# Kernel tuning notes

Measured on AMD Instinct MI355X. Metric: run time of the kernel, lower is better.

## Reference

```python
import jax, jax.numpy as jnp
import numpy as np

N, E = 50000, 500000
DH, DL = 13, 128          # handcrafted / learned node feature dims
OH, OL = 32, 96           # node-encoder output dims; node_dim D = OH+OL
D = OH + OL               # 128
EIN = (DH + DL) + 1 + 3 * D + 1  # 527, forced by concat in forward
H = 256                   # MLP hidden width
HC = 64                   # classifier hidden width
EPS = 1e-8


def _mlp(x, W1, b1, W2, b2):
    # 2-layer MLP with ReLU, matching repo MLP(fc_dims=[H, out])
    return jax.nn.relu(x @ W1 + b1) @ W2 + b2


def _cosine(a, b):
    # torch.nn.CosineSimilarity(dim=1, eps=1e-8)
    na = jnp.maximum(jnp.linalg.norm(a, axis=-1), EPS)
    nb = jnp.maximum(jnp.linalg.norm(b, axis=-1), EPS)
    return jnp.sum(a * b, axis=-1) / (na * nb)


def _lin(key, fan_in, fan_out):
    kW, kb = jax.random.split(key)
    s = 1.0 / np.sqrt(fan_in)
    return (jax.random.uniform(kW, (fan_in, fan_out), jnp.float32, -s, s),
            jax.random.uniform(kb, (fan_out,), jnp.float32, -s, s))


def setup_inputs() -> dict:
    key = jax.random.key(0)
    ks = jax.random.split(key, 16)
    x1 = jax.random.normal(ks[0], (N, DH), jnp.float32)
    x2 = jax.random.normal(ks[1], (N, DL), jnp.float32)
    edge_index = jax.random.randint(ks[2], (2, E), 0, N, jnp.int64)
    Wh1, bh1 = _lin(ks[3], DH, H);   Wh2, bh2 = _lin(ks[4], H, OH)
    Wl1, bl1 = _lin(ks[5], DL, H);   Wl2, bl2 = _lin(ks[6], H, OL)
    We1, be1 = _lin(ks[7], EIN, H);  We2, be2 = _lin(ks[8], H, D)
    Wmsg, bmsg = _lin(ks[9], 2 * D, D)
    Wnode, bnode = _lin(ks[10], 2 * D, D)
    Wmp1, bmp1 = _lin(ks[11], 3 * D, H); Wmp2, bmp2 = _lin(ks[12], H, D)
    Wc1, bc1 = _lin(ks[13], D, HC);  Wc2, bc2 = _lin(ks[14], HC, 1)
    return dict(x1=x1, x2=x2, edge_index=edge_index,
                Wh1=Wh1, bh1=bh1, Wh2=Wh2, bh2=bh2,
                Wl1=Wl1, bl1=bl1, Wl2=Wl2, bl2=bl2,
                We1=We1, be1=be1, We2=We2, be2=be2,
                Wmsg=Wmsg, bmsg=bmsg, Wnode=Wnode, bnode=bnode,
                Wmp1=Wmp1, bmp1=bmp1, Wmp2=Wmp2, bmp2=bmp2,
                Wc1=Wc1, bc1=bc1, Wc2=Wc2, bc2=bc2)


def reference(x1, x2, edge_index,
              Wh1, bh1, Wh2, bh2,
              Wl1, bl1, Wl2, bl2,
              We1, be1, We2, be2,
              Wmsg, bmsg, Wnode, bnode,
              Wmp1, bmp1, Wmp2, bmp2,
              Wc1, bc1, Wc2, bc2):
    src, trg = edge_index[0], edge_index[1]
    # raw-feature edge descriptors
    x_init = jnp.concatenate((x1, x2), axis=-1)            # [N, 141]
    xi_s, xi_t = x_init[src], x_init[trg]                  # gathers [E, 141]
    sim1 = _cosine(xi_s, xi_t)                             # [E]
    abs_init = jnp.abs(xi_s - xi_t)                        # [E, 141]
    # node encoders
    h1 = _mlp(x1, Wh1, bh1, Wh2, bh2)                      # [N, 32]
    h2 = _mlp(x2, Wl1, bl1, Wl2, bl2)                      # [N, 96]
    x = jnp.concatenate((h1, h2), axis=-1)                 # [N, 128]
    xs, xt = x[src], x[trg]                                # [E, 128]
    sim2 = _cosine(xs, xt)                                 # [E]
    edge_feat_in = jnp.concatenate(
        (abs_init, sim1[:, None], xs, xt, jnp.abs(xs - xt), sim2[:, None]),
        axis=-1)                                           # [E, 527]
    e = _mlp(edge_feat_in, We1, be1, We2, be2)             # [E, 128]
    # edge MPNN round: edge->node aggregation, node update, edge update
    msg = jax.nn.relu(jnp.concatenate((xs, e), axis=-1) @ Wmsg + bmsg)  # [E, 128]
    agg = jax.ops.segment_sum(msg, trg, num_segments=N)    # [N, 128]
    xn = jax.nn.relu(jnp.concatenate((x, agg), axis=-1) @ Wnode + bnode)  # [N, 128]
    e_mp = _mlp(jnp.concatenate((xn[src], xn[trg], e), axis=-1),
                Wmp1, bmp1, Wmp2, bmp2)                    # [E, 128]
    pred = _mlp(e_mp, Wc1, bc1, Wc2, bc2)                  # [E, 1]
    return jnp.squeeze(pred, axis=-1)                      # [E]
```

## Files before the change

### kernel.cpp

```cpp
#include <hip/hip_runtime.h>
#include <hip/hip_bf16.h>
#include <hip/hip_fp16.h>


using fp16 = __half;
typedef _Float16 h16;
typedef _Float16 f16x8 __attribute__((ext_vector_type(8)));
typedef _Float16 h16x2 __attribute__((ext_vector_type(2)));
typedef short s16x8 __attribute__((ext_vector_type(8)));
typedef float f32x4 __attribute__((ext_vector_type(4)));

#define NN 50000
#define EE 500000
#define EPSC 1e-8f
#define SCAN_B 196

__device__ __forceinline__ float reluf(float v){ return v > 0.f ? v : 0.f; }

__device__ __forceinline__ float dot8(const f16x8 a, const f16x8 b, float acc)
{
#pragma unroll
  for (int i = 0; i < 4; ++i) {
    const h16x2 av = {a[2 * i], a[2 * i + 1]};
    const h16x2 bv = {b[2 * i], b[2 * i + 1]};
    acc = __builtin_amdgcn_fdot2(av, bv, acc, false);
  }
  return acc;
}

__device__ __forceinline__ f16x8 absdiff8(const f16x8 a, const f16x8 b)
{
  const f16x8 d = a - b;
  s16x8 di = __builtin_bit_cast(s16x8, d);
  di &= (short)0x7fff;
  return __builtin_bit_cast(f16x8, di);
}

#define OFF_E1   0
#define OFF_E2   139264
#define OFF_MSG  172032
#define OFF_NODE 204800
#define OFF_MP1  237568
#define OFF_MP2  335872
#define OFF_C1   368640
#define OFF_N1   376832
#define OFF_N2   458752
#define WT_TOTAL 524288
#define BF_TOTAL 640

__global__ __launch_bounds__(256) void k_prep(
    const float* __restrict__ We1, const float* __restrict__ We2,
    const float* __restrict__ Wmsg, const float* __restrict__ Wnode,
    const float* __restrict__ Wmp1, const float* __restrict__ Wmp2,
    const float* __restrict__ Wc1,
    const float* __restrict__ Wh1, const float* __restrict__ Wl1,
    const float* __restrict__ Wh2, const float* __restrict__ Wl2,
    const float* __restrict__ bh1, const float* __restrict__ bl1,
    const float* __restrict__ bh2, const float* __restrict__ bl2,
    h16* __restrict__ WT, float* __restrict__ BF)
{
  int idx = blockIdx.x * 256 + threadIdx.x;
  if (idx >= WT_TOTAL) {
    const int b = idx - WT_TOTAL;
    if (b < 512) BF[b] = (b < 256) ? bh1[b] : bl1[b - 256];
    else if (b < BF_TOTAL) {
      const int c = b - 512;
      BF[b] = (c < 32) ? bh2[c] : bl2[c - 32];
    }
    return;
  }
  h16 v;
  if (idx < OFF_E2) {
    const int L = idx, n = L / 544, k = L % 544;
    int r;
    if      (k < 128) r = 142 + k;
    else if (k < 256) r = 270 + (k - 128);
    else if (k < 384) r = 398 + (k - 256);
    else if (k < 512) r = 13 + (k - 384);
    else if (k < 525) r = k - 512;
    else if (k == 528) r = 141;
    else if (k == 529) r = 526;
    else r = -1;
    v = (h16)((r >= 0) ? We1[r * 256 + n] : 0.f);
  } else if (idx < OFF_MSG) {
    const int L = idx - OFF_E2, n = L >> 8, k = L & 255;
    v = (h16)We2[k * 128 + n];
  } else if (idx < OFF_NODE) {
    const int L = idx - OFF_MSG, n = L >> 8, k = L & 255;
    const int ko = (k < 128) ? (128 + k) : (k - 128);
    v = (h16)Wmsg[ko * 128 + n];
  } else if (idx < OFF_MP1) {
    const int L = idx - OFF_NODE, n = L >> 8, k = L & 255;
    v = (h16)Wnode[k * 128 + n];
  } else if (idx < OFF_MP2) {
    const int L = idx - OFF_MP1, n = L / 384, k = L % 384;
    v = (h16)Wmp1[k * 256 + n];
  } else if (idx < OFF_C1) {
    const int L = idx - OFF_MP2, n = L >> 8, k = L & 255;
    v = (h16)Wmp2[k * 128 + n];
  } else if (idx < OFF_N1) {
    const int L = idx - OFF_C1, n = L >> 7, k = L & 127;
    v = (h16)Wc1[k * 64 + n];
  } else if (idx < OFF_N2) {
    const int L = idx - OFF_N1, n = L / 160, k = L % 160;
    float f = 0.f;
    if (n < 256) { if (k < 13) f = Wh1[k * 256 + n]; }
    else { if (k >= 16 && k < 144) f = Wl1[(k - 16) * 256 + (n - 256)]; }
    v = (h16)f;
  } else {
    const int L = idx - OFF_N2, n = L >> 9, k = L & 511;
    float f = 0.f;
    if (n < 32) { if (k < 256) f = Wh2[k * 32 + n]; }
    else { if (k >= 256) f = Wl2[(k - 256) * 96 + (n - 32)]; }
    v = (h16)f;
  }
  WT[idx] = v;
}

__global__ __launch_bounds__(256) void k_cvt(
    const float* __restrict__ x1, const float* __restrict__ x2,
    const int* __restrict__ ei,
    h16* __restrict__ X1P, h16* __restrict__ X2H, int* __restrict__ CNT)
{
  const int idx = blockIdx.x * 256 + threadIdx.x;
  if (idx < EE) atomicAdd(&CNT[ei[EE + idx]], 1);
  if (idx < NN * 16) {
    const int nn = idx >> 4, j = idx & 15;
    X1P[idx] = (h16)((j < 13) ? x1[nn * 13 + j] : 0.f);
  }
  const int i2 = idx - NN * 16;
  if (i2 >= 0 && i2 < NN * 128) X2H[i2] = (h16)x2[i2];
}

__global__ __launch_bounds__(256) void k_scanA(
    const int* __restrict__ CNT, int* __restrict__ TEX, int* __restrict__ BS)
{
  __shared__ int sd[256];
  const int tid = threadIdx.x;
  const int i = blockIdx.x * 256 + tid;
  const int v = (i < NN) ? CNT[i] : 0;
  sd[tid] = v;
  __syncthreads();
  for (int off = 1; off < 256; off <<= 1) {
    const int x = (tid >= off) ? sd[tid - off] : 0;
    __syncthreads();
    sd[tid] += x;
    __syncthreads();
  }
  if (i < NN) TEX[i] = sd[tid] - v;
  if (tid == 255) BS[blockIdx.x] = sd[255];
}

__global__ __launch_bounds__(256) void k_scanB(
    const int* __restrict__ BS, int* __restrict__ BSSE)
{
  __shared__ int sd[256];
  const int tid = threadIdx.x;
  const int v = (tid < SCAN_B) ? BS[tid] : 0;
  sd[tid] = v;
  __syncthreads();
  for (int off = 1; off < 256; off <<= 1) {
    const int x = (tid >= off) ? sd[tid - off] : 0;
    __syncthreads();
    sd[tid] += x;
    __syncthreads();
  }
  if (tid < SCAN_B) BSSE[tid] = sd[tid] - v;
}

__global__ __launch_bounds__(256) void k_scatter(
    const int* __restrict__ ei, const int* __restrict__ TEX,
    const int* __restrict__ BSSE, int* __restrict__ POS,
    int* __restrict__ ES, int* __restrict__ ET, int* __restrict__ OID)
{
  const int e = blockIdx.x * 256 + threadIdx.x;
  if (e >= EE) return;
  const int t = ei[EE + e];
  const int p = atomicAdd(&POS[t], 1);
  const int idx = BSSE[t >> 8] + TEX[t] + p;
  ES[idx] = ei[e];
  ET[idx] = t;
  OID[idx] = e;
}

template<int ROWS, int UDIM, int KP, int LDA, int WAVES, int RS, bool RELU,
         bool ENDSYNC, typename F>
__device__ __forceinline__ void mfma_gemm(const h16* sA,
    const h16* __restrict__ WT, const float* __restrict__ bias, F emit)
{
  constexpr int CS = WAVES / RS;
  constexpr int RG = ROWS / RS;
  constexpr int RT = RG / 16;
  constexpr int NPW0 = UDIM / CS;
  constexpr int NPW = (NPW0 < 16) ? 16 : NPW0;
  constexpr int NT = NPW / 16;
  constexpr int NSTEPS = KP / 32;
  constexpr int CH0 = (NT >= 8) ? 1 : ((NT >= 4) ? 2 : 4);
  constexpr int CHUNK = (NSTEPS < CH0) ? NSTEPS : CH0;
  constexpr int NCH = (NSTEPS + CHUNK - 1) / CHUNK;
  const int tid = threadIdx.x;
  const int wave = tid >> 6;
  const int lane = tid & 63;
  const int m = lane & 15;
  const int quad = lane >> 4;
  const int wr = wave % RS;
  const int wc = wave / RS;
  const int rbase = wr * RG;
  const int n0 = wc * NPW;
  const bool active = (n0 < UDIM);

  f32x4 acc[RT][NT];
#pragma unroll
  for (int r = 0; r < RT; ++r)
#pragma unroll
    for (int j = 0; j < NT; ++j) acc[r][j] = (f32x4){0.f, 0.f, 0.f, 0.f};
  float bb[NT];

  if (active) {
    const h16* wbase = &WT[(size_t)(n0 + m) * KP + quad * 8];
#pragma unroll
    for (int j = 0; j < NT; ++j) bb[j] = bias[n0 + j * 16 + m];

    f16x8 breg[2][CHUNK][NT];
#pragma unroll
    for (int s = 0; s < CHUNK; ++s)
      if (s < NSTEPS)
#pragma unroll
        for (int j = 0; j < NT; ++j)
          breg[0][s][j] = *(const f16x8*)&wbase[(size_t)j * 16 * KP + s * 32];
    asm volatile("" ::: "memory");

#pragma unroll
    for (int c = 0; c < NCH; ++c) {
      if (c + 1 < NCH) {
#pragma unroll
        for (int s = 0; s < CHUNK; ++s) {
          const int st = (c + 1) * CHUNK + s;
          if (st < NSTEPS)
#pragma unroll
            for (int j = 0; j < NT; ++j)
              breg[(c + 1) & 1][s][j] =
                  *(const f16x8*)&wbase[(size_t)j * 16 * KP + st * 32];
        }
      }
#pragma unroll
      for (int s = 0; s < CHUNK; ++s) {
        const int st = c * CHUNK + s;
        if (st < NSTEPS) {
          const int k0 = st * 32;
#pragma unroll
          for (int r = 0; r < RT; ++r) {
            const f16x8 af = *(const f16x8*)&sA[(rbase + r * 16 + m) * LDA + k0 + quad * 8];
#pragma unroll
            for (int j = 0; j < NT; ++j)
              acc[r][j] = __builtin_amdgcn_mfma_f32_16x16x32_f16(af, breg[c & 1][s][j], acc[r][j], 0, 0, 0);
          }
        }
      }
      asm volatile("" ::: "memory");
    }
  }
  __syncthreads();
  if (active) {
#pragma unroll
    for (int j = 0; j < NT; ++j) {
      const int col = n0 + j * 16 + m;
#pragma unroll
      for (int r = 0; r < RT; ++r)
#pragma unroll
        for (int g = 0; g < 4; ++g) {
          const int row = rbase + r * 16 + quad * 4 + g;
          float v = acc[r][j][g] + bb[j];
          if (RELU) v = reluf(v);
          emit(row, col, v);
        }
    }
  }
  if (ENDSYNC) __syncthreads();
}

__global__ __launch_bounds__(512, 4) void k_nenc(
    const h16* __restrict__ X1P, const h16* __restrict__ X2H,
    const h16* __restrict__ WT, const float* __restrict__ BF,
    h16* __restrict__ XH)
{
  __shared__ __align__(16) h16 sA[32 * 168];
  __shared__ __align__(16) h16 sH[32 * 520];
  const int tid = threadIdx.x;
  const int n0 = blockIdx.x * 32;
  const int remn = NN - n0;
  const int cnt = remn < 32 ? remn : 32;
  const int n = tid >> 4;
  const int q = tid & 15;

  if (n < cnt) {
    const int node = n0 + n;
    if (q < 2)
      *(f16x8*)&sA[n * 168 + q * 8] = *(const f16x8*)&X1P[node * 16 + q * 8];
    else if (q < 4)
      *(f16x8*)&sA[n * 168 + 144 + (q - 2) * 8] = (f16x8){};
    *(f16x8*)&sA[n * 168 + 16 + q * 8] =
        *(const f16x8*)&X2H[(size_t)node * 128 + q * 8];
  }
  __syncthreads();

  mfma_gemm<32, 512, 160, 168, 8, 1, true, true>(sA, WT + OFF_N1, BF,
      [&](int row, int col, float v) { sH[row * 520 + col] = (h16)v; });
  mfma_gemm<32, 128, 512, 520, 8, 1, false, false>(sH, WT + OFF_N2, BF + 512,
      [&](int row, int col, float v) {
        if (row < cnt) XH[(size_t)(n0 + row) * 128 + col] = (h16)v;
      });
}

__global__ __launch_bounds__(512, 4) void k_edge_mlp(
    const h16* __restrict__ X1P, const h16* __restrict__ X2H,
    const int* __restrict__ ES, const int* __restrict__ ET,
    const h16* __restrict__ XH, const h16* __restrict__ WT,
    const float* __restrict__ be1, const float* __restrict__ be2,
    const float* __restrict__ bmsg,
    h16* __restrict__ EB, float* __restrict__ AGG)
{
  __shared__ __align__(16) h16 sFeat[64 * 568];
  __shared__ int strg[64];
  const int tid = threadIdx.x;
  const long e0 = (long)blockIdx.x * 64;
  const long rem = (long)EE - e0;
  const int cnt = rem < 64 ? (int)rem : 64;
  const int n = tid >> 3;
  const int q = tid & 7;
  h16* Arow = &sFeat[n * 568];
  f16x8 xsv0 = {}, xsv1 = {};

  if (n < cnt) {
    const int s = ES[e0 + n];
    const int t = ET[e0 + n];
    if (q == 0) strg[n] = t;
    float ds = 0.f, ns = 0.f, nt = 0.f;
    if (q < 2) {
      const f16x8 a = *(const f16x8*)&X1P[s * 16 + q * 8];
      const f16x8 b = *(const f16x8*)&X1P[t * 16 + q * 8];
      ds = dot8(a, b, ds); ns = dot8(a, a, ns); nt = dot8(b, b, nt);
      *(f16x8*)&Arow[512 + q * 8] = absdiff8(a, b);
    }
#pragma unroll
    for (int c = 0; c < 2; ++c) {
      const f16x8 a = *(const f16x8*)&X2H[(size_t)s * 128 + q * 16 + c * 8];
      const f16x8 b = *(const f16x8*)&X2H[(size_t)t * 128 + q * 16 + c * 8];
      ds = dot8(a, b, ds); ns = dot8(a, a, ns); nt = dot8(b, b, nt);
      *(f16x8*)&Arow[384 + q * 16 + c * 8] = absdiff8(a, b);
    }
    ds += __shfl_xor(ds, 1); ds += __shfl_xor(ds, 2); ds += __shfl_xor(ds, 4);
    ns += __shfl_xor(ns, 1); ns += __shfl_xor(ns, 2); ns += __shfl_xor(ns, 4);
    nt += __shfl_xor(nt, 1); nt += __shfl_xor(nt, 2); nt += __shfl_xor(nt, 4);
    if (q == 0)
      Arow[528] = (h16)(ds / (fmaxf(sqrtf(ns), EPSC) * fmaxf(sqrtf(nt), EPSC)));

    float ds2 = 0.f, ns2 = 0.f, nt2 = 0.f;
#pragma unroll
    for (int c = 0; c < 2; ++c) {
      const f16x8 a = *(const f16x8*)&XH[(size_t)s * 128 + q * 16 + c * 8];
      const f16x8 b = *(const f16x8*)&XH[(size_t)t * 128 + q * 16 + c * 8];
      if (c == 0) xsv0 = a; else xsv1 = a;
      ds2 = dot8(a, b, ds2); ns2 = dot8(a, a, ns2); nt2 = dot8(b, b, nt2);
      *(f16x8*)&Arow[q * 16 + c * 8]       = a;
      *(f16x8*)&Arow[128 + q * 16 + c * 8] = b;
      *(f16x8*)&Arow[256 + q * 16 + c * 8] = absdiff8(a, b);
    }
    ds2 += __shfl_xor(ds2, 1); ds2 += __shfl_xor(ds2, 2); ds2 += __shfl_xor(ds2, 4);
    ns2 += __shfl_xor(ns2, 1); ns2 += __shfl_xor(ns2, 2); ns2 += __shfl_xor(ns2, 4);
    nt2 += __shfl_xor(nt2, 1); nt2 += __shfl_xor(nt2, 2); nt2 += __shfl_xor(nt2, 4);
    if (q == 0)
      Arow[529] = (h16)(ds2 / (fmaxf(sqrtf(ns2), EPSC) * fmaxf(sqrtf(nt2), EPSC)));
    for (int j = 530 + q; j < 544; j += 8) Arow[j] = (h16)0.f;
  } else {
    if (q == 0) strg[n] = 0;
    for (int j8 = q; j8 < 71; j8 += 8) *(f16x8*)&Arow[j8 * 8] = (f16x8){};
  }
  __syncthreads();

  h16* sHid = sFeat;
  mfma_gemm<64, 256, 544, 568, 8, 1, true, true>(sFeat, WT + OFF_E1, be1,
      [&](int row, int col, float v) { sHid[row * 264 + col] = (h16)v; });
  mfma_gemm<64, 128, 256, 264, 8, 1, false, false>(sHid, WT + OFF_E2, be2,
      [&](int row, int col, float v) {
        const h16 vh = (h16)v;
        if (row < cnt) EB[(size_t)(e0 + row) * 128 + col] = vh;
        sHid[row * 264 + col] = vh;
      });
  *(f16x8*)&sFeat[n * 264 + 128 + q * 16]     = xsv0;
  *(f16x8*)&sFeat[n * 264 + 128 + q * 16 + 8] = xsv1;
  __syncthreads();
  mfma_gemm<64, 128, 256, 264, 8, 1, true, true>(sFeat, WT + OFF_MSG, bmsg,
      [&](int row, int col, float v) {
        *(float*)((char*)sFeat + row * 528 + col * 4) = v;
      });
  {
    const int c = tid & 127;
    const int g = tid >> 7;
    const int r0 = g * 16;
    if (r0 < cnt) {
      const int rend = (r0 + 16 < cnt) ? r0 + 16 : cnt;
      float acc = 0.f;
      int cur = strg[r0];
      for (int r = r0; r < rend; ++r) {
        const int t = strg[r];
        if (t != cur) {
          atomicAdd(&AGG[(size_t)cur * 128 + c], acc);
          acc = 0.f; cur = t;
        }
        acc += *(const float*)((const char*)sFeat + r * 528 + c * 4);
      }
      atomicAdd(&AGG[(size_t)cur * 128 + c], acc);
    }
  }
}

__global__ __launch_bounds__(256, 4) void k_node_update(
    const h16* __restrict__ XH, const float* __restrict__ AGG,
    const h16* __restrict__ WT, const float* __restrict__ bnode,
    h16* __restrict__ XNH)
{
  __shared__ __align__(16) h16 sA[64 * 264];
  const int tid = threadIdx.x;
  const int n0 = blockIdx.x * 64;
  const int remn = NN - n0;
  const int cnt = remn < 64 ? remn : 64;
  const int n = tid >> 2;
  const int q = tid & 3;

  if (n < cnt) {
    const f16x8* xr = (const f16x8*)&XH[(size_t)(n0 + n) * 128];
    const float4* ar = (const float4*)&AGG[(size_t)(n0 + n) * 128];
    for (int j8 = q; j8 < 16; j8 += 4)
      *(f16x8*)&sA[n * 264 + j8 * 8] = xr[j8];
    for (int j4 = q; j4 < 32; j4 += 4) {
      const float4 b = ar[j4];
      h16* p1 = &sA[n * 264 + 128 + j4 * 4];
      p1[0] = (h16)b.x; p1[1] = (h16)b.y; p1[2] = (h16)b.z; p1[3] = (h16)b.w;
    }
  } else {
    for (int j = q; j < 256; j += 4) sA[n * 264 + j] = (h16)0.f;
  }
  __syncthreads();

  mfma_gemm<64, 128, 256, 264, 4, 1, true, false>(sA, WT + OFF_NODE, bnode,
      [&](int row, int col, float v) {
        if (row < cnt) XNH[(size_t)(n0 + row) * 128 + col] = (h16)v;
      });
}

__global__ __launch_bounds__(1024, 4) void k_empl(
    const int* __restrict__ ES, const int* __restrict__ ET,
    const int* __restrict__ OID, const h16* __restrict__ XNH,
    const h16* __restrict__ EB, const h16* __restrict__ WT,
    const float* __restrict__ bmp1, const float* __restrict__ bmp2,
    const float* __restrict__ bc1,
    const float* __restrict__ Wc2, const float* __restrict__ bc2,
    float* __restrict__ out)
{
  __shared__ __align__(16) h16 sF[128 * 392];
  const int tid = threadIdx.x;
  const long e0 = (long)blockIdx.x * 128;
  const long rem = (long)EE - e0;
  const int cnt = rem < 128 ? (int)rem : 128;
  const int n = tid >> 3;
  const int q = tid & 7;

  if (n < cnt) {
    const int s = ES[e0 + n];
    const int t = ET[e0 + n];
    const f16x8* xsr = (const f16x8*)&XNH[(size_t)s * 128];
    const f16x8* xtr = (const f16x8*)&XNH[(size_t)t * 128];
    const f16x8* ebr = (const f16x8*)&EB[(size_t)(e0 + n) * 128];
#pragma unroll
    for (int j8 = q; j8 < 16; j8 += 8) {
      *(f16x8*)&sF[n * 392 + j8 * 8]       = xsr[j8];
      *(f16x8*)&sF[n * 392 + 128 + j8 * 8] = xtr[j8];
      *(f16x8*)&sF[n * 392 + 256 + j8 * 8] = ebr[j8];
    }
  } else {
    for (int j8 = q; j8 < 49; j8 += 8) *(f16x8*)&sF[n * 392 + j8 * 8] = (f16x8){};
  }
  __syncthreads();

  h16*  sH2 = sF;
  h16*  sE  = sF;
  float* sHC = (float*)((char*)sF + 34816);
  mfma_gemm<128, 256, 384, 392, 16, 1, true, true>(sF, WT + OFF_MP1, bmp1,
      [&](int row, int col, float v) { sH2[row * 264 + col] = (h16)v; });
  mfma_gemm<128, 128, 256, 264, 16, 1, false, true>(sH2, WT + OFF_MP2, bmp2,
      [&](int row, int col, float v) { sE[row * 136 + col] = (h16)v; });
  mfma_gemm<128, 64, 128, 136, 16, 1, true, true>(sE, WT + OFF_C1, bc1,
      [&](int row, int col, float v) { sHC[row * 65 + col] = v; });
  if (tid < cnt) {
    float acc = bc2[0];
    for (int k = 0; k < 64; ++k) acc += sHC[tid * 65 + k] * Wc2[k];
    out[OID[e0 + tid]] = acc;
  }
}

extern "C" void kernel_launch(void* const* d_in, const int* in_sizes, int n_in,
                              void* d_out, int out_size, void* d_ws, size_t ws_size,
                              hipStream_t stream)
{
  const float* x1  = (const float*)d_in[0];
  const float* x2  = (const float*)d_in[1];
  const int*   ei  = (const int*)d_in[2];
  const float* Wh1 = (const float*)d_in[3],  *bh1 = (const float*)d_in[4];
  const float* Wh2 = (const float*)d_in[5],  *bh2 = (const float*)d_in[6];
  const float* Wl1 = (const float*)d_in[7],  *bl1 = (const float*)d_in[8];
  const float* Wl2 = (const float*)d_in[9],  *bl2 = (const float*)d_in[10];
  const float* We1 = (const float*)d_in[11], *be1 = (const float*)d_in[12];
  const float* We2 = (const float*)d_in[13], *be2 = (const float*)d_in[14];
  const float* Wmsg = (const float*)d_in[15], *bmsg = (const float*)d_in[16];
  const float* Wnode = (const float*)d_in[17], *bnode = (const float*)d_in[18];
  const float* Wmp1 = (const float*)d_in[19], *bmp1 = (const float*)d_in[20];
  const float* Wmp2 = (const float*)d_in[21], *bmp2 = (const float*)d_in[22];
  const float* Wc1 = (const float*)d_in[23], *bc1 = (const float*)d_in[24];
  const float* Wc2 = (const float*)d_in[25], *bc2 = (const float*)d_in[26];
  float* out = (float*)d_out;

  float* AGG = (float*)d_ws;
  h16*   EB  = (h16*)(AGG + (size_t)NN * 128);
  h16*   WT  = EB + (size_t)EE * 128;
  h16*   XH  = WT + WT_TOTAL;
  h16*   XNH = XH + (size_t)NN * 128;
  h16*   X1P = XNH + (size_t)NN * 128;
  h16*   X2H = X1P + (size_t)NN * 16;
  float* BF  = (float*)(X2H + (size_t)NN * 128);
  int*   CNT = (int*)(BF + BF_TOTAL);
  int*   POS = CNT + NN;
  int*   TEX = POS + NN;
  int*   ES  = TEX + NN;
  int*   ET  = ES + EE;
  int*   OID = ET + EE;
  int*   BS  = OID + EE;
  int*   BSSE = BS + 256;

  k_prep<<<(WT_TOTAL + BF_TOTAL + 255) / 256, 256, 0, stream>>>(
      We1, We2, Wmsg, Wnode, Wmp1, Wmp2, Wc1,
      Wh1, Wl1, Wh2, Wl2, bh1, bl1, bh2, bl2, WT, BF);
  hipMemsetAsync(AGG, 0, (size_t)NN * 128 * sizeof(float), stream);
  hipMemsetAsync(CNT, 0, (size_t)2 * NN * sizeof(int), stream);
  k_cvt<<<(NN * 16 + NN * 128 + 255) / 256, 256, 0, stream>>>(
      x1, x2, ei, X1P, X2H, CNT);
  k_scanA<<<SCAN_B, 256, 0, stream>>>(CNT, TEX, BS);
  k_scanB<<<1, 256, 0, stream>>>(BS, BSSE);
  k_scatter<<<(EE + 255) / 256, 256, 0, stream>>>(ei, TEX, BSSE, POS, ES, ET, OID);
  k_nenc<<<(NN + 31) / 32, 512, 0, stream>>>(X1P, X2H, WT, BF, XH);
  k_edge_mlp<<<7813, 512, 0, stream>>>(X1P, X2H, ES, ET, XH, WT,
                                       be1, be2, bmsg, EB, AGG);
  k_node_update<<<782, 256, 0, stream>>>(XH, AGG, WT, bnode, XNH);
  k_empl<<<3907, 1024, 0, stream>>>(ES, ET, OID, XNH, EB, WT, bmp1, bmp2, bc1,
                                    Wc2, bc2, out);
}
```

Measured before the change: 850.7 us.

## Make edge MLP kernel persistent with register prefetch of next tile's gathers

Launches the edge MLP kernel with a fixed grid of 512 blocks that loop over edge tiles. The random gathers for the next tile (node features for source and target) are issued into registers before the aggregation atomics of the current tile, to overlap gather latency with compute. This adds register pressure and an extra barrier per tile. It also reduces the number of resident blocks, which may lower occupancy-based latency hiding.

Result: slower. 1.022 ms (+20.1%).

```diff
diff --git a/kernel.cpp b/kernel.cpp
--- a/kernel.cpp
+++ b/kernel.cpp
@@ -14,6 +14,8 @@
 #define EE 500000
 #define EPSC 1e-8f
 #define SCAN_B 196
+#define NTILES 7813
+#define PGRID 512
 
 __device__ __forceinline__ float reluf(float v){ return v > 0.f ? v : 0.f; }
 
@@ -323,95 +325,119 @@
   __shared__ __align__(16) h16 sFeat[64 * 568];
   __shared__ int strg[64];
   const int tid = threadIdx.x;
-  const long e0 = (long)blockIdx.x * 64;
-  const long rem = (long)EE - e0;
-  const int cnt = rem < 64 ? (int)rem : 64;
   const int n = tid >> 3;
   const int q = tid & 7;
   h16* Arow = &sFeat[n * 568];
-  f16x8 xsv0 = {}, xsv1 = {};
-
-  if (n < cnt) {
-    const int s = ES[e0 + n];
-    const int t = ET[e0 + n];
-    if (q == 0) strg[n] = t;
-    float ds = 0.f, ns = 0.f, nt = 0.f;
+
+  int pt = 0;
+  f16x8 p1a = {}, p1b = {};
+  f16x8 p2a0 = {}, p2a1 = {}, p2b0 = {}, p2b1 = {};
+  f16x8 pha0 = {}, pha1 = {}, phb0 = {}, phb1 = {};
+
+  auto issue = [&](long tl) {
+    const long e0 = tl * 64;
+    const long rem = (long)EE - e0;
+    const int cnt = rem < 64 ? (int)rem : 64;
+    int s = 0, t = 0;
+    if (n < cnt) { s = ES[e0 + n]; t = ET[e0 + n]; }
+    pt = t;
     if (q < 2) {
-      const f16x8 a = *(const f16x8*)&X1P[s * 16 + q * 8];
-      const f16x8 b = *(const f16x8*)&X1P[t * 16 + q * 8];
-      ds = dot8(a, b, ds); ns = dot8(a, a, ns); nt = dot8(b, b, nt);
-      *(f16x8*)&Arow[512 + q * 8] = absdiff8(a, b);
-    }
-#pragma unroll
-    for (int c = 0; c < 2; ++c) {
-      const f16x8 a = *(const f16x8*)&X2H[(size_t)s * 128 + q * 16 + c * 8];
-      const f16x8 b = *(const f16x8*)&X2H[(size_t)t * 128 + q * 16 + c * 8];
-      ds = dot8(a, b, ds); ns = dot8(a, a, ns); nt = dot8(b, b, nt);
-      *(f16x8*)&Arow[384 + q * 16 + c * 8] = absdiff8(a, b);
-    }
-    ds += __shfl_xor(ds, 1); ds += __shfl_xor(ds, 2); ds += __shfl_xor(ds, 4);
-    ns += __shfl_xor(ns, 1); ns += __shfl_xor(ns, 2); ns += __shfl_xor(ns, 4);
-    nt += __shfl_xor(nt, 1); nt += __shfl_xor(nt, 2); nt += __shfl_xor(nt, 4);
-    if (q == 0)
-      Arow[528] = (h16)(ds / (fmaxf(sqrtf(ns), EPSC) * fmaxf(sqrtf(nt), EPSC)));
-
-    float ds2 = 0.f, ns2 = 0.f, nt2 = 0.f;
-#pragma unroll
-    for (int c = 0; c < 2; ++c) {
-      const f16x8 a = *(const f16x8*)&XH[(size_t)s * 128 + q * 16 + c * 8];
-      const f16x8 b = *(const f16x8*)&XH[(size_t)t * 128 + q * 16 + c * 8];
-      if (c == 0) xsv0 = a; else xsv1 = a;
-      ds2 = dot8(a, b, ds2); ns2 = dot8(a, a, ns2); nt2 = dot8(b, b, nt2);
-      *(f16x8*)&Arow[q * 16 + c * 8]       = a;
-      *(f16x8*)&Arow[128 + q * 16 + c * 8] = b;
-      *(f16x8*)&Arow[256 + q * 16 + c * 8] = absdiff8(a, b);
-    }
-    ds2 += __shfl_xor(ds2, 1); ds2 += __shfl_xor(ds2, 2); ds2 += __shfl_xor(ds2, 4);
-    ns2 += __shfl_xor(ns2, 1); ns2 += __shfl_xor(ns2, 2); ns2 += __shfl_xor(ns2, 4);
-    nt2 += __shfl_xor(nt2, 1); nt2 += __shfl_xor(nt2, 2); nt2 += __shfl_xor(nt2, 4);
-    if (q == 0)
-      Arow[529] = (h16)(ds2 / (fmaxf(sqrtf(ns2), EPSC) * fmaxf(sqrtf(nt2), EPSC)));
-    for (int j = 530 + q; j < 544; j += 8) Arow[j] = (h16)0.f;
-  } else {
-    if (q == 0) strg[n] = 0;
-    for (int j8 = q; j8 < 71; j8 += 8) *(f16x8*)&Arow[j8 * 8] = (f16x8){};
-  }
-  __syncthreads();
-
-  h16* sHid = sFeat;
-  mfma_gemm<64, 256, 544, 568, 8, 1, true, true>(sFeat, WT + OFF_E1, be1,
-      [&](int row, int col, float v) { sHid[row * 264 + col] = (h16)v; });
-  mfma_gemm<64, 128, 256, 264, 8, 1, false, false>(sHid, WT + OFF_E2, be2,
-      [&](int row, int col, float v) {
-        const h16 vh = (h16)v;
-        if (row < cnt) EB[(size_t)(e0 + row) * 128 + col] = vh;
-        sHid[row * 264 + col] = vh;
-      });
-  *(f16x8*)&sFeat[n * 264 + 128 + q * 16]     = xsv0;
-  *(f16x8*)&sFeat[n * 264 + 128 + q * 16 + 8] = xsv1;
-  __syncthreads();
-  mfma_gemm<64, 128, 256, 264, 8, 1, true, true>(sFeat, WT + OFF_MSG, bmsg,
-      [&](int row, int col, float v) {
-        *(float*)((char*)sFeat + row * 528 + col * 4) = v;
-      });
-  {
-    const int c = tid & 127;
-    const int g = tid >> 7;
-    const int r0 = g * 16;
-    if (r0 < cnt) {
-      const int rend = (r0 + 16 < cnt) ? r0 + 16 : cnt;
-      float acc = 0.f;
-      int cur = strg[r0];
-      for (int r = r0; r < rend; ++r) {
-        const int t = strg[r];
-        if (t != cur) {
-          atomicAdd(&AGG[(size_t)cur * 128 + c], acc);
-          acc = 0.f; cur = t;
+      p1a = *(const f16x8*)&X1P[s * 16 + q * 8];
+      p1b = *(const f16x8*)&X1P[t * 16 + q * 8];
+    }
+    p2a0 = *(const f16x8*)&X2H[(size_t)s * 128 + q * 16];
+    p2a1 = *(const f16x8*)&X2H[(size_t)s * 128 + q * 16 + 8];
+    p2b0 = *(const f16x8*)&X2H[(size_t)t * 128 + q * 16];
+    p2b1 = *(const f16x8*)&X2H[(size_t)t * 128 + q * 16 + 8];
+    pha0 = *(const f16x8*)&XH[(size_t)s * 128 + q * 16];
+    pha1 = *(const f16x8*)&XH[(size_t)s * 128 + q * 16 + 8];
+    phb0 = *(const f16x8*)&XH[(size_t)t * 128 + q * 16];
+    phb1 = *(const f16x8*)&XH[(size_t)t * 128 + q * 16 + 8];
+  };
+
+  long tile = blockIdx.x;
+  issue(tile);
+
+  for (; tile < NTILES; tile += PGRID) {
+    const long e0 = tile * 64;
+    const long rem = (long)EE - e0;
+    const int cnt = rem < 64 ? (int)rem : 64;
+
+    if (n < cnt) {
+      if (q == 0) strg[n] = pt;
+      float ds = 0.f, ns = 0.f, nt = 0.f;
+      if (q < 2) {
+        ds = dot8(p1a, p1b, ds); ns = dot8(p1a, p1a, ns); nt = dot8(p1b, p1b, nt);
+        *(f16x8*)&Arow[512 + q * 8] = absdiff8(p1a, p1b);
+      }
+      ds = dot8(p2a0, p2b0, ds); ns = dot8(p2a0, p2a0, ns); nt = dot8(p2b0, p2b0, nt);
+      *(f16x8*)&Arow[384 + q * 16] = absdiff8(p2a0, p2b0);
+      ds = dot8(p2a1, p2b1, ds); ns = dot8(p2a1, p2a1, ns); nt = dot8(p2b1, p2b1, nt);
+      *(f16x8*)&Arow[384 + q * 16 + 8] = absdiff8(p2a1, p2b1);
+      ds += __shfl_xor(ds, 1); ds += __shfl_xor(ds, 2); ds += __shfl_xor(ds, 4);
+      ns += __shfl_xor(ns, 1); ns += __shfl_xor(ns, 2); ns += __shfl_xor(ns, 4);
+      nt += __shfl_xor(nt, 1); nt += __shfl_xor(nt, 2); nt += __shfl_xor(nt, 4);
+      if (q == 0)
+        Arow[528] = (h16)(ds / (fmaxf(sqrtf(ns), EPSC) * fmaxf(sqrtf(nt), EPSC)));
+
+      float ds2 = 0.f, ns2 = 0.f, nt2 = 0.f;
+      ds2 = dot8(pha0, phb0, ds2); ns2 = dot8(pha0, pha0, ns2); nt2 = dot8(phb0, phb0, nt2);
+      *(f16x8*)&Arow[q * 16]       = pha0;
+      *(f16x8*)&Arow[128 + q * 16] = phb0;
+      *(f16x8*)&Arow[256 + q * 16] = absdiff8(pha0, phb0);
+      ds2 = dot8(pha1, phb1, ds2); ns2 = dot8(pha1, pha1, ns2); nt2 = dot8(phb1, phb1, nt2);
+      *(f16x8*)&Arow[q * 16 + 8]       = pha1;
+      *(f16x8*)&Arow[128 + q * 16 + 8] = phb1;
+      *(f16x8*)&Arow[256 + q * 16 + 8] = absdiff8(pha1, phb1);
+      ds2 += __shfl_xor(ds2, 1); ds2 += __shfl_xor(ds2, 2); ds2 += __shfl_xor(ds2, 4);
+      ns2 += __shfl_xor(ns2, 1); ns2 += __shfl_xor(ns2, 2); ns2 += __shfl_xor(ns2, 4);
+      nt2 += __shfl_xor(nt2, 1); nt2 += __shfl_xor(nt2, 2); nt2 += __shfl_xor(nt2, 4);
+      if (q == 0)
+        Arow[529] = (h16)(ds2 / (fmaxf(sqrtf(ns2), EPSC) * fmaxf(sqrtf(nt2), EPSC)));
+      for (int j = 530 + q; j < 544; j += 8) Arow[j] = (h16)0.f;
+    } else {
+      if (q == 0) strg[n] = 0;
+      for (int j8 = q; j8 < 71; j8 += 8) *(f16x8*)&Arow[j8 * 8] = (f16x8){};
+    }
+    __syncthreads();
+
+    h16* sHid = sFeat;
+    mfma_gemm<64, 256, 544, 568, 8, 1, true, true>(sFeat, WT + OFF_E1, be1,
+        [&](int row, int col, float v) { sHid[row * 264 + col] = (h16)v; });
+    mfma_gemm<64, 128, 256, 264, 8, 1, false, false>(sHid, WT + OFF_E2, be2,
+        [&](int row, int col, float v) {
+          const h16 vh = (h16)v;
+          if (row < cnt) EB[(size_t)(e0 + row) * 128 + col] = vh;
+          sHid[row * 264 + col] = vh;
+        });
+    *(f16x8*)&sFeat[n * 264 + 128 + q * 16]     = pha0;
+    *(f16x8*)&sFeat[n * 264 + 128 + q * 16 + 8] = pha1;
+    __syncthreads();
+    mfma_gemm<64, 128, 256, 264, 8, 1, true, true>(sFeat, WT + OFF_MSG, bmsg,
+        [&](int row, int col, float v) {
+          *(float*)((char*)sFeat + row * 528 + col * 4) = v;
+        });
+    if (tile + PGRID < NTILES) issue(tile + PGRID);
+    {
+      const int c = tid & 127;
+      const int g = tid >> 7;
+      const int r0 = g * 16;
+      if (r0 < cnt) {
+        const int rend = (r0 + 16 < cnt) ? r0 + 16 : cnt;
+        float acc = 0.f;
+        int cur = strg[r0];
+        for (int r = r0; r < rend; ++r) {
+          const int t = strg[r];
+          if (t != cur) {
+            atomicAdd(&AGG[(size_t)cur * 128 + c], acc);
+            acc = 0.f; cur = t;
+          }
+          acc += *(const float*)((const char*)sFeat + r * 528 + c * 4);
         }
-        acc += *(const float*)((const char*)sFeat + r * 528 + c * 4);
+        atomicAdd(&AGG[(size_t)cur * 128 + c], acc);
       }
-      atomicAdd(&AGG[(size_t)cur * 128 + c], acc);
-    }
+    }
+    __syncthreads();
   }
 }
 
@@ -548,8 +574,8 @@
   k_scanB<<<1, 256, 0, stream>>>(BS, BSSE);
   k_scatter<<<(EE + 255) / 256, 256, 0, stream>>>(ei, TEX, BSSE, POS, ES, ET, OID);
   k_nenc<<<(NN + 31) / 32, 512, 0, stream>>>(X1P, X2H, WT, BF, XH);
-  k_edge_mlp<<<7813, 512, 0, stream>>>(X1P, X2H, ES, ET, XH, WT,
-                                       be1, be2, bmsg, EB, AGG);
+  k_edge_mlp<<<PGRID, 512, 0, stream>>>(X1P, X2H, ES, ET, XH, WT,
+                                        be1, be2, bmsg, EB, AGG);
   k_node_update<<<782, 256, 0, stream>>>(XH, AGG, WT, bnode, XNH);
   k_empl<<<3907, 1024, 0, stream>>>(ES, ET, OID, XNH, EB, WT, bmp1, bmp2, bc1,
                                     Wc2, bc2, out);
```
